# Kernel optimization log

Measured on AMD Instinct MI355X. Metric: run time of the kernel, lower is better.

Reference implementation:

```python
import jax, jax.numpy as jnp
import numpy as np

B, C, H, W, O, K = 4, 64, 128, 128, 64, 3


def setup_inputs() -> dict:
    key = jax.random.key(0)
    kx, ko, kw = jax.random.split(key, 3)
    x = jax.random.normal(kx, (B, C, H, W), dtype=jnp.float32)
    offset = jax.random.normal(ko, (B, 2 * K * K, H, W), dtype=jnp.float32)
    stdv = 1.0 / np.sqrt(C * K * K)
    weight = jax.random.uniform(kw, (O, C, K, K), dtype=jnp.float32,
                                minval=-stdv, maxval=stdv)
    return {"x": x, "offset": offset, "weight": weight}


def _deform_conv(x, offset, weight):
    b, c, h, w = x.shape
    o = weight.shape[0]
    k = weight.shape[2]
    kk = k * k
    # kernel tap displacements, flattened row-major (ki*K + kj), centered at 0
    taps = jnp.arange(k) - k // 2
    di = jnp.repeat(taps, k)            # [kk]
    dj = jnp.tile(taps, k)              # [kk]
    # base sampling coords: base_i[h,1,kk], base_j[1,w,kk]
    base_i = (jnp.arange(h)[:, None, None] + di).astype(jnp.float32)
    base_j = (jnp.arange(w)[None, :, None] + dj).astype(jnp.float32)
    # offset: [b, kk, 2, h, w] -> [b, h, w, kk, 2]
    off = offset.reshape(b, kk, 2, h, w).transpose(0, 3, 4, 1, 2)
    ci = off[..., 0] + base_i           # [b,h,w,kk] float sample row coords
    cj = off[..., 1] + base_j           # [b,h,w,kk] float sample col coords

    i_lt = jnp.floor(ci).astype(jnp.int32)
    i_rb = jnp.ceil(ci).astype(jnp.int32)
    j_lt = jnp.floor(cj).astype(jnp.int32)
    j_rb = jnp.ceil(cj).astype(jnp.int32)

    def gather(ii, jj):
        # out-of-bounds samples contribute 0 (matching the torch masking)
        inb = (ii >= 0) & (ii < h) & (jj >= 0) & (jj < w)
        ic = jnp.clip(ii, 0, h - 1)
        jc = jnp.clip(jj, 0, w - 1)
        # per-image gather: xb[:, i, j] with i,j of shape [h,w,kk] -> [c,h,w,kk]
        v = jax.vmap(lambda xb, i, j: xb[:, i, j])(x, ic, jc)  # [b,c,h,w,kk]
        return v * inb[:, None].astype(x.dtype)

    vals_lt = gather(i_lt, j_lt)
    vals_rb = gather(i_rb, j_rb)
    vals_rt = gather(i_lt, j_rb)
    vals_lb = gather(i_rb, j_lt)

    # fractional parts (gradient flows to offset only through these)
    fi = (ci - i_lt.astype(ci.dtype))[:, None]   # [b,1,h,w,kk]
    fj = (cj - j_lt.astype(cj.dtype))[:, None]

    vals_t = vals_lt + fj * (vals_rt - vals_lt)
    vals_b = vals_lb + fj * (vals_rb - vals_lb)
    mapped = vals_t + fi * (vals_b - vals_t)     # [b,c,h,w,kk]

    # final GEMM: weight [o, c*kk] x im2col-like [c*kk, b*h*w]
    return jnp.einsum('ock,bchwk->bohw', weight.reshape(o, c, kk), mapped)


def reference(x, offset, weight):
    return _deform_conv(x, offset, weight)
```

## Files before the change

kernel.cpp:

```cpp
#include <hip/hip_runtime.h>

namespace {
constexpr int B = 4, C = 64, H = 128, W = 128, O = 64, KK = 9;
constexpr int PREPT = 256;
constexpr int MAINT = 512;
constexpr int WF_ELEMS = KK * 2 * 4 * 64 * 8;
constexpr size_t XT_BYTES = (size_t)B * H * W * C * 2;
constexpr size_t WF_BYTES = (size_t)WF_ELEMS * 2;
constexpr size_t WS_NEED  = XT_BYTES + WF_BYTES;
}

typedef float    f32x4 __attribute__((ext_vector_type(4)));
typedef _Float16 f16x2 __attribute__((ext_vector_type(2)));
typedef _Float16 f16x8 __attribute__((ext_vector_type(8)));

__device__ __forceinline__ unsigned hpack2(float a, float b) {
  f16x2 v; v[0] = (_Float16)a; v[1] = (_Float16)b;
  return __builtin_bit_cast(unsigned, v);
}
__device__ __forceinline__ void gload16(const void* g, void* l) {
  __builtin_amdgcn_global_load_lds(
      (const __attribute__((address_space(1))) unsigned*)g,
      (__attribute__((address_space(3))) unsigned*)l, 16, 0, 0);
}

__global__ __launch_bounds__(PREPT)
void prep_fused(const float* __restrict__ x, const float* __restrict__ wgt,
                unsigned* __restrict__ xt_u32, unsigned short* __restrict__ wf) {
  __shared__ float st[64][65];
  const int t = threadIdx.x;

  const int gid = blockIdx.x * PREPT + t;
  if (gid < WF_ELEMS) {
    const int e = gid & 7, lane = (gid >> 3) & 63, mt = (gid >> 9) & 3;
    const int ks = (gid >> 11) & 1, tap = gid >> 12;
    const int o = mt * 16 + (lane & 15);
    const int c = ks * 32 + ((lane >> 4) << 3) + e;
    const _Float16 hv = (_Float16)wgt[(size_t)o * (C * KK) + c * KK + tap];
    wf[gid] = __builtin_bit_cast(unsigned short, hv);
  }

  const int half = blockIdx.x & 1, h = (blockIdx.x >> 1) & 127, b = blockIdx.x >> 8;
  const int w0 = half * 64;
#pragma unroll
  for (int it = 0; it < 16; ++it) {
    const int w = t & 63, c = it * 4 + (t >> 6);
    st[w][c] = x[((size_t)(b * C + c) * H + h) * W + w0 + w];
  }
  __syncthreads();
#pragma unroll
  for (int it = 0; it < 8; ++it) {
    const int idx = it * PREPT + t;
    const int w = idx >> 5, c2 = (idx & 31) * 2;
    xt_u32[(size_t)(((b * H + h) * W) + w0 + w) * 32 + (c2 >> 1)] = hpack2(st[w][c2], st[w][c2 + 1]);
  }
}

__global__ __launch_bounds__(MAINT) __attribute__((amdgpu_waves_per_eu(4)))
void deform_mfma(const float* __restrict__ offs, const char* __restrict__ xt,
                 const char* __restrict__ wfg, float* __restrict__ out) {
  __shared__ unsigned short s_wf[2][4096];
  __shared__ unsigned short s_m[128 * 64];
  __shared__ unsigned s_pw[8][KK][16][2];
  __shared__ unsigned s_pa[8][KK][16][4];

  const int t = threadIdx.x, l = t & 63, wid = t >> 6;
  const int nid = (blockIdx.x & 7) * 64 + (blockIdx.x >> 3);
  const int h = nid & 127, b = nid >> 7;
  const int wbase = wid * 16;

#pragma unroll
  for (int it = 0; it < 3; ++it) {
    const int item = it * 64 + l;
    if (item < KK * 16) {
      const int tap = item >> 4, pix = item & 15;
      const int ki = tap / 3, kj = tap - ki * 3;
      const int w = wbase + pix;
      const float* ob = offs + ((size_t)b * (2 * KK) + 2 * tap) * (H * W) + h * W + w;
      const float oi = ob[0], oj = ob[H * W];
      const float ci = oi + (float)(h + ki - 1);
      const float cj = oj + (float)(w + kj - 1);
      const float fli = floorf(ci), flj = floorf(cj);
      const int i0 = (int)fli, j0 = (int)flj, i1 = i0 + 1, j1 = j0 + 1;
      const float fi = ci - fli, fj = cj - flj, gi = 1.f - fi, gj = 1.f - fj;
      const bool bi0 = (unsigned)i0 < (unsigned)H, bi1 = (unsigned)i1 < (unsigned)H;
      const bool bj0 = (unsigned)j0 < (unsigned)W, bj1 = (unsigned)j1 < (unsigned)W;
      const int ic0 = min(max(i0, 0), H - 1), ic1 = min(max(i1, 0), H - 1);
      const int jc0 = min(max(j0, 0), W - 1), jc1 = min(max(j1, 0), W - 1);
      const float w00 = gi * gj * (float)(bi0 && bj0);
      const float w01 = gi * fj * (float)(bi0 && bj1);
      const float w10 = fi * gj * (float)(bi1 && bj0);
      const float w11 = fi * fj * (float)(bi1 && bj1);
      s_pw[wid][tap][pix][0] = hpack2(w00, w01);
      s_pw[wid][tap][pix][1] = hpack2(w10, w11);
      s_pa[wid][tap][pix][0] = (unsigned)(((b * H + ic0) * W + jc0) << 7);
      s_pa[wid][tap][pix][1] = (unsigned)(((b * H + ic0) * W + jc1) << 7);
      s_pa[wid][tap][pix][2] = (unsigned)(((b * H + ic1) * W + jc0) << 7);
      s_pa[wid][tap][pix][3] = (unsigned)(((b * H + ic1) * W + jc1) << 7);
    }
  }

  const int pix8 = l >> 3, oct = l & 7, cb = oct << 4;

  char* smb = (char*)s_m;
  const int wb  = ((wid * 16 + pix8) << 7) + ((oct ^ pix8) << 4);
  const int rr  = wid * 16 + (l & 15);
  const int rd0 = (rr << 7) + ((((l >> 4)    ) ^ (l & 7)) << 4);
  const int rd1 = (rr << 7) + (((4 + (l >> 4)) ^ (l & 7)) << 4);

  f32x4 acc[4];
#pragma unroll
  for (int mt = 0; mt < 4; ++mt) acc[mt] = (f32x4)0.f;

  uint4 g[2][4];
#define ISSUE(TAPX, HS) do {                                                   \
    const uint4 ad = *(const uint4*)&s_pa[wid][(TAPX)][(HS) * 8 + pix8][0];    \
    g[HS][0] = *(const uint4*)(xt + ad.x + cb);                                \
    g[HS][1] = *(const uint4*)(xt + ad.y + cb);                                \
    g[HS][2] = *(const uint4*)(xt + ad.z + cb);                                \
    g[HS][3] = *(const uint4*)(xt + ad.w + cb);                                \
  } while (0)

#define LERPH(c0_, c1_, c2_, c3_) __builtin_bit_cast(unsigned, (f16x2)(        \
    __builtin_bit_cast(f16x2, c0_) * W00 + __builtin_bit_cast(f16x2, c1_) * W01 + \
    __builtin_bit_cast(f16x2, c2_) * W10 + __builtin_bit_cast(f16x2, c3_) * W11))

#define STAGE(TAPV, HS) do {                                                   \
    const uint2 pk = *(const uint2*)&s_pw[wid][(TAPV)][(HS) * 8 + pix8][0];    \
    const f16x2 pa_ = __builtin_bit_cast(f16x2, pk.x);                         \
    const f16x2 pb_ = __builtin_bit_cast(f16x2, pk.y);                         \
    const f16x2 W00 = {pa_[0], pa_[0]}, W01 = {pa_[1], pa_[1]};                \
    const f16x2 W10 = {pb_[0], pb_[0]}, W11 = {pb_[1], pb_[1]};                \
    uint4* gc = g[HS];                                                         \
    uint4 r;                                                                   \
    r.x = LERPH(gc[0].x, gc[1].x, gc[2].x, gc[3].x);                           \
    r.y = LERPH(gc[0].y, gc[1].y, gc[2].y, gc[3].y);                           \
    r.z = LERPH(gc[0].z, gc[1].z, gc[2].z, gc[3].z);                           \
    r.w = LERPH(gc[0].w, gc[1].w, gc[2].w, gc[3].w);                           \
    *(uint4*)(smb + wb + (HS) * 1024) = r;                                     \
  } while (0)

  gload16(wfg + (size_t)t * 16, (char*)s_wf + t * 16);
  ISSUE(0, 0);
  ISSUE(0, 1);

#pragma unroll 1
  for (int tap = 0; tap < KK; ++tap) {
    __syncthreads();

    if (tap + 1 < KK) {
      gload16(wfg + (size_t)(tap + 1) * 8192 + t * 16,
              (char*)s_wf + ((tap + 1) & 1) * 8192 + t * 16);
    }

    STAGE(tap, 0);
    if (tap + 1 < KK) ISSUE(tap + 1, 0);
    STAGE(tap, 1);
    if (tap + 1 < KK) ISSUE(tap + 1, 1);

    const char* wl = (const char*)s_wf + (tap & 1) * 8192;
    const f16x8 b0 = *(const f16x8*)(smb + rd0);
    const f16x8 b1 = *(const f16x8*)(smb + rd1);
#pragma unroll
    for (int mt = 0; mt < 4; ++mt) {
      const f16x8 a0 = *(const f16x8*)(wl + mt * 1024 + l * 16);
      acc[mt] = __builtin_amdgcn_mfma_f32_16x16x32_f16(a0, b0, acc[mt], 0, 0, 0);
    }
#pragma unroll
    for (int mt = 0; mt < 4; ++mt) {
      const f16x8 a1 = *(const f16x8*)(wl + 4096 + mt * 1024 + l * 16);
      acc[mt] = __builtin_amdgcn_mfma_f32_16x16x32_f16(a1, b1, acc[mt], 0, 0, 0);
    }
  }
#undef ISSUE
#undef LERPH
#undef STAGE

#pragma unroll
  for (int mt = 0; mt < 4; ++mt)
#pragma unroll
    for (int j = 0; j < 4; ++j) {
      const int o = mt * 16 + ((l >> 4) << 2) + j;
      out[((size_t)(b * O + o) * H + h) * W + wbase + (l & 15)] = acc[mt][j];
    }
}

namespace fb {
constexpr int WT = 32, CH = 16, NCHUNK = 4, KC = 144, WPAD = 68;
}
__global__ __launch_bounds__(PREPT, 2)
void deform_conv_fused(const float* __restrict__ x, const float* __restrict__ offs,
                       const float* __restrict__ wgt, float* __restrict__ out) {
  using namespace fb;
  __shared__ int   s_i0[KK][WT];
  __shared__ int   s_j0[KK][WT];
  __shared__ float s_fi[KK][WT];
  __shared__ float s_fj[KK][WT];
  __shared__ float s_w[KC][WPAD];
  __shared__ float s_m[KC][WT + 1];
  const int t = threadIdx.x;
  const int nwt = W / WT;
  const int wt = blockIdx.x % nwt, h = (blockIdx.x / nwt) % H, b = blockIdx.x / (nwt * H);
  const int w0 = wt * WT;
  for (int idx = t; idx < KK * WT; idx += PREPT) {
    const int k = idx / WT, p = idx % WT, w = w0 + p;
    const float oi = offs[(((size_t)b * (2 * KK) + 2 * k) * H + h) * W + w];
    const float oj = offs[(((size_t)b * (2 * KK) + 2 * k + 1) * H + h) * W + w];
    const float ci = oi + (float)(h + (k / 3) - 1), cj = oj + (float)(w + (k % 3) - 1);
    const float fli = floorf(ci), flj = floorf(cj);
    s_i0[k][p] = (int)fli; s_j0[k][p] = (int)flj;
    s_fi[k][p] = ci - fli; s_fj[k][p] = cj - flj;
  }
  float acc[8];
#pragma unroll
  for (int i = 0; i < 8; ++i) acc[i] = 0.f;
  const int p = t & (WT - 1), ob = (t >> 5) * 8;
  for (int cc = 0; cc < NCHUNK; ++cc) {
    const int c0 = cc * CH;
    __syncthreads();
    for (int idx = t; idx < O * KC; idx += PREPT)
      s_w[idx % KC][idx / KC] = wgt[(size_t)(idx / KC) * (C * KK) + (size_t)c0 * KK + idx % KC];
    for (int idx = t; idx < CH * KK * WT; idx += PREPT) {
      const int pp = idx & (WT - 1), rest = idx >> 5, k = rest % KK, cl = rest / KK;
      const int i0 = s_i0[k][pp], j0 = s_j0[k][pp], i1 = i0 + 1, j1 = j0 + 1;
      const float fi = s_fi[k][pp], fj = s_fj[k][pp];
      const float* xb = x + (size_t)(b * C + c0 + cl) * H * W;
      const float v00 = ((unsigned)i0 < (unsigned)H && (unsigned)j0 < (unsigned)W) ? xb[i0 * W + j0] : 0.f;
      const float v01 = ((unsigned)i0 < (unsigned)H && (unsigned)j1 < (unsigned)W) ? xb[i0 * W + j1] : 0.f;
      const float v10 = ((unsigned)i1 < (unsigned)H && (unsigned)j0 < (unsigned)W) ? xb[i1 * W + j0] : 0.f;
      const float v11 = ((unsigned)i1 < (unsigned)H && (unsigned)j1 < (unsigned)W) ? xb[i1 * W + j1] : 0.f;
      const float top = v00 + fj * (v01 - v00), bot = v10 + fj * (v11 - v10);
      s_m[cl * KK + k][pp] = top + fi * (bot - top);
    }
    __syncthreads();
#pragma unroll 4
    for (int k = 0; k < KC; ++k) {
      const float a = s_m[k][p];
      const float4 wv0 = *reinterpret_cast<const float4*>(&s_w[k][ob]);
      const float4 wv1 = *reinterpret_cast<const float4*>(&s_w[k][ob + 4]);
      acc[0] += a * wv0.x; acc[1] += a * wv0.y; acc[2] += a * wv0.z; acc[3] += a * wv0.w;
      acc[4] += a * wv1.x; acc[5] += a * wv1.y; acc[6] += a * wv1.z; acc[7] += a * wv1.w;
    }
  }
#pragma unroll
  for (int i = 0; i < 8; ++i)
    out[(((size_t)b * O + ob + i) * H + h) * W + w0 + p] = acc[i];
}

extern "C" void kernel_launch(void* const* d_in, const int* in_sizes, int n_in,
                              void* d_out, int out_size, void* d_ws, size_t ws_size,
                              hipStream_t stream) {
  const float* x    = (const float*)d_in[0];
  const float* offs = (const float*)d_in[1];
  const float* wgt  = (const float*)d_in[2];
  float* out = (float*)d_out;

  if (ws_size < WS_NEED) {
    deform_conv_fused<<<B * H * (W / 32), PREPT, 0, stream>>>(x, offs, wgt, out);
    return;
  }
  char* xt = (char*)d_ws;
  unsigned short* wf = (unsigned short*)(xt + XT_BYTES);

  prep_fused<<<B * H * 2, PREPT, 0, stream>>>(x, wgt, (unsigned*)xt, wf);
  deform_mfma<<<B * H, MAINT, 0, stream>>>(offs, xt, (const char*)wf, out);
}
```

Measured before the change: 30.31 us.

## Process two taps per barrier and pack bilinear sample coordinates into one word

The tap loop now covers two taps per iteration. The weight tiles for a pair are prefetched together into a double buffer that grows from two to four LDS tap slots, so block barriers drop from nine to five. The four precomputed gather addresses per sample are replaced by one packed 32-bit word holding the clamped row and column indices, which cuts LDS footprint and reads at the cost of a few extra bit operations per issue. MFMA sections are wrapped in s_setprio to favour the matrix instructions. The trade-off is more LDS for weights and longer intervals between barriers, which could affect occupancy or latency hiding.

```diff
diff --git a/kernel.cpp b/kernel.cpp
--- a/kernel.cpp
+++ b/kernel.cpp
@@ -59,10 +59,10 @@
 __global__ __launch_bounds__(MAINT) __attribute__((amdgpu_waves_per_eu(4)))
 void deform_mfma(const float* __restrict__ offs, const char* __restrict__ xt,
                  const char* __restrict__ wfg, float* __restrict__ out) {
-  __shared__ unsigned short s_wf[2][4096];
+  __shared__ unsigned short s_wf[4][4096];
   __shared__ unsigned short s_m[128 * 64];
   __shared__ unsigned s_pw[8][KK][16][2];
-  __shared__ unsigned s_pa[8][KK][16][4];
+  __shared__ unsigned s_pp[8][KK][16];
 
   const int t = threadIdx.x, l = t & 63, wid = t >> 6;
   const int nid = (blockIdx.x & 7) * 64 + (blockIdx.x >> 3);
@@ -93,16 +93,16 @@
       const float w11 = fi * fj * (float)(bi1 && bj1);
       s_pw[wid][tap][pix][0] = hpack2(w00, w01);
       s_pw[wid][tap][pix][1] = hpack2(w10, w11);
-      s_pa[wid][tap][pix][0] = (unsigned)(((b * H + ic0) * W + jc0) << 7);
-      s_pa[wid][tap][pix][1] = (unsigned)(((b * H + ic0) * W + jc1) << 7);
-      s_pa[wid][tap][pix][2] = (unsigned)(((b * H + ic1) * W + jc0) << 7);
-      s_pa[wid][tap][pix][3] = (unsigned)(((b * H + ic1) * W + jc1) << 7);
+      s_pp[wid][tap][pix] = (unsigned)jc0 | ((unsigned)ic0 << 7) |
+                            ((unsigned)jc1 << 14) | ((unsigned)ic1 << 21);
     }
   }
 
   const int pix8 = l >> 3, oct = l & 7, cb = oct << 4;
+  const char* xb = xt + ((size_t)b * H * W << 7) + cb;
 
   char* smb = (char*)s_m;
+  char* smw = (char*)s_wf;
   const int wb  = ((wid * 16 + pix8) << 7) + ((oct ^ pix8) << 4);
   const int rr  = wid * 16 + (l & 15);
   const int rd0 = (rr << 7) + ((((l >> 4)    ) ^ (l & 7)) << 4);
@@ -114,11 +114,15 @@
 
   uint4 g[2][4];
 #define ISSUE(TAPX, HS) do {                                                   \
-    const uint4 ad = *(const uint4*)&s_pa[wid][(TAPX)][(HS) * 8 + pix8][0];    \
-    g[HS][0] = *(const uint4*)(xt + ad.x + cb);                                \
-    g[HS][1] = *(const uint4*)(xt + ad.y + cb);                                \
-    g[HS][2] = *(const uint4*)(xt + ad.z + cb);                                \
-    g[HS][3] = *(const uint4*)(xt + ad.w + cb);                                \
+    const unsigned v_ = s_pp[wid][(TAPX)][(HS) * 8 + pix8];                    \
+    const unsigned i0s = v_ & 0x3F80u;                                         \
+    const unsigned j0_ = v_ & 0x7Fu;                                           \
+    const unsigned j1_ = (v_ >> 14) & 0x7Fu;                                   \
+    const unsigned i1s = (v_ >> 14) & 0x3F80u;                                 \
+    g[HS][0] = *(const uint4*)(xb + ((size_t)(i0s | j0_) << 7));               \
+    g[HS][1] = *(const uint4*)(xb + ((size_t)(i0s | j1_) << 7));               \
+    g[HS][2] = *(const uint4*)(xb + ((size_t)(i1s | j0_) << 7));               \
+    g[HS][3] = *(const uint4*)(xb + ((size_t)(i1s | j1_) << 7));               \
   } while (0)
 
 #define LERPH(c0_, c1_, c2_, c3_) __builtin_bit_cast(unsigned, (f16x2)(        \
@@ -140,41 +144,53 @@
     *(uint4*)(smb + wb + (HS) * 1024) = r;                                     \
   } while (0)
 
-  gload16(wfg + (size_t)t * 16, (char*)s_wf + t * 16);
+#define DO_TAP(TAPV, WL) do {                                                  \
+    STAGE(TAPV, 0);                                                            \
+    if ((TAPV) + 1 < KK) ISSUE((TAPV) + 1, 0);                                 \
+    STAGE(TAPV, 1);                                                            \
+    if ((TAPV) + 1 < KK) ISSUE((TAPV) + 1, 1);                                 \
+    const f16x8 b0 = *(const f16x8*)(smb + rd0);                               \
+    const f16x8 b1 = *(const f16x8*)(smb + rd1);                               \
+    __builtin_amdgcn_s_setprio(1);                                             \
+    _Pragma("unroll")                                                          \
+    for (int mt = 0; mt < 4; ++mt) {                                           \
+      const f16x8 a0 = *(const f16x8*)((WL) + mt * 1024 + l * 16);             \
+      acc[mt] = __builtin_amdgcn_mfma_f32_16x16x32_f16(a0, b0, acc[mt], 0, 0, 0); \
+    }                                                                          \
+    _Pragma("unroll")                                                          \
+    for (int mt = 0; mt < 4; ++mt) {                                           \
+      const f16x8 a1 = *(const f16x8*)((WL) + 4096 + mt * 1024 + l * 16);      \
+      acc[mt] = __builtin_amdgcn_mfma_f32_16x16x32_f16(a1, b1, acc[mt], 0, 0, 0); \
+    }                                                                          \
+    __builtin_amdgcn_s_setprio(0);                                             \
+  } while (0)
+
+  gload16(wfg + (size_t)t * 16, smw + t * 16);
+  gload16(wfg + 8192 + (size_t)t * 16, smw + 8192 + t * 16);
   ISSUE(0, 0);
   ISSUE(0, 1);
 
 #pragma unroll 1
-  for (int tap = 0; tap < KK; ++tap) {
+  for (int pair = 0; pair < 5; ++pair) {
+    const int t0 = pair * 2;
     __syncthreads();
 
-    if (tap + 1 < KK) {
-      gload16(wfg + (size_t)(tap + 1) * 8192 + t * 16,
-              (char*)s_wf + ((tap + 1) & 1) * 8192 + t * 16);
-    }
-
-    STAGE(tap, 0);
-    if (tap + 1 < KK) ISSUE(tap + 1, 0);
-    STAGE(tap, 1);
-    if (tap + 1 < KK) ISSUE(tap + 1, 1);
-
-    const char* wl = (const char*)s_wf + (tap & 1) * 8192;
-    const f16x8 b0 = *(const f16x8*)(smb + rd0);
-    const f16x8 b1 = *(const f16x8*)(smb + rd1);
-#pragma unroll
-    for (int mt = 0; mt < 4; ++mt) {
-      const f16x8 a0 = *(const f16x8*)(wl + mt * 1024 + l * 16);
-      acc[mt] = __builtin_amdgcn_mfma_f32_16x16x32_f16(a0, b0, acc[mt], 0, 0, 0);
-    }
-#pragma unroll
-    for (int mt = 0; mt < 4; ++mt) {
-      const f16x8 a1 = *(const f16x8*)(wl + 4096 + mt * 1024 + l * 16);
-      acc[mt] = __builtin_amdgcn_mfma_f32_16x16x32_f16(a1, b1, acc[mt], 0, 0, 0);
-    }
+    if (pair < 4) {
+      const int n0 = t0 + 2;
+      char* dst = smw + ((pair + 1) & 1) * 16384;
+      gload16(wfg + (size_t)n0 * 8192 + t * 16, dst + t * 16);
+      if (n0 + 1 < KK)
+        gload16(wfg + (size_t)(n0 + 1) * 8192 + t * 16, dst + 8192 + t * 16);
+    }
+
+    const char* wl0 = smw + (pair & 1) * 16384;
+    DO_TAP(t0, wl0);
+    if (t0 + 1 < KK) DO_TAP(t0 + 1, wl0 + 8192);
   }
 #undef ISSUE
 #undef LERPH
 #undef STAGE
+#undef DO_TAP
 
 #pragma unroll
   for (int mt = 0; mt < 4; ++mt)
```

New measurement: 29.73 us. About the same (-1.9%).
